# Kernel optimization log

Hardware: AMD Instinct MI355X
Metric: run time of the kernel (lower is better)

## Reference

```python
import jax, jax.numpy as jnp
import numpy as np

N_HEADS = 8
D_K = 64
SCALE = D_K ** (-0.5)


def setup_inputs() -> dict:
    key = jax.random.key(0)
    k1, k2, k3 = jax.random.split(key, 3)
    B, C, H, W = 8, 512, 32, 32
    x = jax.random.normal(k1, (B, C, H, W), dtype=jnp.float32)
    # Linear weights stored as [in, out] so y = x @ W + b (same math as torch Linear)
    W_qkv = jax.random.normal(k2, (C, N_HEADS * D_K * 3), dtype=jnp.float32) * (1.0 / np.sqrt(C))
    b_qkv = jnp.zeros((N_HEADS * D_K * 3,), dtype=jnp.float32)
    W_out = jax.random.normal(k3, (N_HEADS * D_K, C), dtype=jnp.float32) * (1.0 / np.sqrt(N_HEADS * D_K))
    b_out = jnp.zeros((C,), dtype=jnp.float32)
    return {"x": x, "W_qkv": W_qkv, "b_qkv": b_qkv, "W_out": W_out, "b_out": b_out}


def reference(x, W_qkv, b_qkv, W_out, b_out):
    B, C, H, W = x.shape
    N = H * W
    # [B, C, H, W] -> [B, N, C]  (tokens are spatial positions)
    xf = jnp.transpose(x.reshape(B, C, N), (0, 2, 1))
    # NOTE: the original forward never applies self.norm, so neither do we.
    qkv = xf @ W_qkv + b_qkv                       # [B, N, 3*h*d]
    qkv = qkv.reshape(B, N, N_HEADS, 3 * D_K)
    q, k, v = jnp.split(qkv, 3, axis=-1)           # each [B, N, h, d]
    attn = jnp.einsum('bihd,bjhd->bijh', q, k) * SCALE
    attn = jax.nn.softmax(attn, axis=2)            # softmax over key index j
    res = jnp.einsum('bijh,bjhd->bihd', attn, v)   # [B, N, h, d]
    res = res.reshape(B, N, N_HEADS * D_K)
    res = res @ W_out + b_out
    res = res + xf                                 # residual
    res = jnp.transpose(res, (0, 2, 1)).reshape(B, C, H, W)
    return res
```

## Files before the change

### kernel.cpp

```cpp
#include <hip/hip_runtime.h>
#include <hip/hip_bf16.h>
#include <cstdint>

typedef __bf16 bf16;
typedef __attribute__((ext_vector_type(8))) __bf16 bf16x8;
typedef __attribute__((ext_vector_type(4))) __bf16 bf16x4;
typedef __attribute__((ext_vector_type(4))) float f32x4;

#define CEXP 0.1803368801111244f

__global__ __launch_bounds__(256) void prep_k(const float* __restrict__ x,
                                              const float* __restrict__ Wqkv,
                                              const float* __restrict__ Wout,
                                              bf16* __restrict__ xT,
                                              bf16* __restrict__ WqkvT,
                                              bf16* __restrict__ WoutT) {
  __shared__ bf16 t[32][33];
  const int z = blockIdx.z;
  const float* src;
  bf16* dst;
  int R, C;
  if (z < 8) {
    if (blockIdx.x >= 32) return;
    src = x + (size_t)z * 512 * 1024;
    dst = xT + (size_t)z * 1024 * 512;
    R = 512; C = 1024;
  } else if (z == 8) {
    src = Wqkv; dst = WqkvT; R = 512; C = 1536;
  } else {
    if (blockIdx.x >= 16) return;
    src = Wout; dst = WoutT; R = 512; C = 512;
  }
  const int c0 = blockIdx.x * 32, r0 = blockIdx.y * 32;
  const int tx = threadIdx.x, ty = threadIdx.y;
#pragma unroll
  for (int i = 0; i < 4; ++i)
    t[ty + i * 8][tx] = (bf16)src[(size_t)(r0 + ty + i * 8) * C + c0 + tx];
  __syncthreads();
#pragma unroll
  for (int i = 0; i < 4; ++i)
    dst[(size_t)(c0 + ty + i * 8) * R + r0 + tx] = t[tx][ty + i * 8];
}

__global__ __launch_bounds__(256) void gemm_qkv(const bf16* __restrict__ xT,
                                                const bf16* __restrict__ WqkvT,
                                                const float* __restrict__ bqkv,
                                                bf16* __restrict__ Qb,
                                                bf16* __restrict__ Kb,
                                                bf16* __restrict__ Vb) {
  __shared__ bf16 As[128 * 64];
  __shared__ bf16 Bs[128 * 64];
  const int b = blockIdx.z;
  const int m0 = blockIdx.y * 128;
  const int co0 = blockIdx.x * 128;
  const int tid = threadIdx.x;
  const int w = tid >> 6, l = tid & 63;
  const int wr = w >> 1, wc = w & 1;
  const int quad = l >> 4, l16 = l & 15;

  const bf16* A = xT + (size_t)b * 1024 * 512;

  f32x4 acc[4][4];
#pragma unroll
  for (int i = 0; i < 4; ++i)
#pragma unroll
    for (int j = 0; j < 4; ++j) acc[i][j] = (f32x4){0.f, 0.f, 0.f, 0.f};

  const int srow = w * 32 + (l >> 3);
  const int scol = (l & 7) * 8;

  for (int kk = 0; kk < 8; ++kk) {
    const int k0 = kk * 64;
    bf16x8 av[4], bv[4];
#pragma unroll
    for (int i = 0; i < 4; ++i) {
      av[i] = *(const bf16x8*)&A[(size_t)(m0 + srow + i * 8) * 512 + k0 + scol];
      bv[i] = *(const bf16x8*)&WqkvT[(size_t)(co0 + srow + i * 8) * 512 + k0 + scol];
    }
#pragma unroll
    for (int i = 0; i < 4; ++i) {
      *(bf16x8*)&As[(srow + i * 8) * 64 + scol] = av[i];
      *(bf16x8*)&Bs[(srow + i * 8) * 64 + scol] = bv[i];
    }
    __syncthreads();
#pragma unroll
    for (int ks = 0; ks < 2; ++ks) {
      bf16x8 a[4], bb[4];
#pragma unroll
      for (int rb = 0; rb < 4; ++rb)
        a[rb] = *(const bf16x8*)&As[(wr * 64 + rb * 16 + l16) * 64 + ks * 32 + quad * 8];
#pragma unroll
      for (int cb = 0; cb < 4; ++cb)
        bb[cb] = *(const bf16x8*)&Bs[(wc * 64 + cb * 16 + l16) * 64 + ks * 32 + quad * 8];
#pragma unroll
      for (int rb = 0; rb < 4; ++rb)
#pragma unroll
        for (int cb = 0; cb < 4; ++cb)
          acc[rb][cb] = __builtin_amdgcn_mfma_f32_16x16x32_bf16(a[rb], bb[cb], acc[rb][cb], 0, 0, 0);
    }
    __syncthreads();
  }

#pragma unroll
  for (int cb = 0; cb < 4; ++cb) {
    const int co = co0 + wc * 64 + cb * 16 + l16;
    const int h = co / 192;
    const int rem = co - h * 192;
    const int part = rem >> 6;
    const int dd = rem & 63;
    const float bias = bqkv[co];
    if (part == 2) {
      bf16* base = Vb + ((size_t)(b * 8 + h) * 64 + dd) * 1024;
#pragma unroll
      for (int rb = 0; rb < 4; ++rb) {
        const int n = m0 + wr * 64 + rb * 16 + quad * 4;
        f32x4 v = acc[rb][cb];
        bf16x4 ov;
#pragma unroll
        for (int r = 0; r < 4; ++r) ov[r] = (bf16)(v[r] + bias);
        *(bf16x4*)&base[n] = ov;
      }
    } else {
      const float sc = (part == 0) ? CEXP : 1.0f;
      bf16* dst = (part == 0) ? Qb : Kb;
      bf16* base = dst + ((size_t)(b * 8 + h) * 1024) * 64 + dd;
#pragma unroll
      for (int rb = 0; rb < 4; ++rb) {
        const int n = m0 + wr * 64 + rb * 16 + quad * 4;
        f32x4 v = acc[rb][cb];
#pragma unroll
        for (int r = 0; r < 4; ++r) base[(size_t)(n + r) * 64] = (bf16)((v[r] + bias) * sc);
      }
    }
  }
}

__global__ __launch_bounds__(256) void attn_k(const bf16* __restrict__ Qb,
                                              const bf16* __restrict__ Kb,
                                              const bf16* __restrict__ Vb,
                                              bf16* __restrict__ Ob) {
  __shared__ bf16 Ks[128 * 72];
  __shared__ bf16 Vs[64 * 136];
  __shared__ bf16 PQs[64 * 136];
  const int bh = blockIdx.x;
  const int b = bh >> 3, h = bh & 7;
  const int q0 = blockIdx.y * 64;
  const int tid = threadIdx.x;
  const int w = tid >> 6, l = tid & 63;
  const int quad = l >> 4, l16 = l & 15;

  const bf16* Qg = Qb + (size_t)bh * 1024 * 64;
  const bf16* Kg = Kb + (size_t)bh * 1024 * 64;
  const bf16* Vg = Vb + (size_t)bh * 64 * 1024;

  {
    const int r = tid >> 2, c = (tid & 3) * 16;
    bf16x8 v0 = *(const bf16x8*)&Qg[(size_t)(q0 + r) * 64 + c];
    bf16x8 v1 = *(const bf16x8*)&Qg[(size_t)(q0 + r) * 64 + c + 8];
    *(bf16x8*)&PQs[r * 72 + c] = v0;
    *(bf16x8*)&PQs[r * 72 + c + 8] = v1;
  }
  __syncthreads();
  bf16x8 qb[4][2];
#pragma unroll
  for (int nb = 0; nb < 4; ++nb)
#pragma unroll
    for (int ks = 0; ks < 2; ++ks)
      qb[nb][ks] = *(const bf16x8*)&PQs[(nb * 16 + l16) * 72 + ks * 32 + quad * 8];

  bf16x8 ones;
#pragma unroll
  for (int e = 0; e < 8; ++e) ones[e] = (bf16)1.0f;

  f32x4 o[4], acc_l = (f32x4){0.f, 0.f, 0.f, 0.f};
#pragma unroll
  for (int db = 0; db < 4; ++db) o[db] = (f32x4){0.f, 0.f, 0.f, 0.f};

  const int kr = tid >> 1, kc = (tid & 1) * 32;
  const int vr = tid >> 2, vc = (tid & 3) * 32;

  bf16x8 ka[4], va[4];
#pragma unroll
  for (int e = 0; e < 4; ++e) {
    ka[e] = *(const bf16x8*)&Kg[(size_t)kr * 64 + kc + e * 8];
    va[e] = *(const bf16x8*)&Vg[(size_t)vr * 1024 + vc + e * 8];
  }

  for (int kv = 0; kv < 8; ++kv) {
    __syncthreads();
#pragma unroll
    for (int e = 0; e < 4; ++e) {
      *(bf16x8*)&Ks[kr * 72 + kc + e * 8] = ka[e];
      *(bf16x8*)&Vs[vr * 136 + vc + e * 8] = va[e];
    }
    __syncthreads();
    if (kv < 7) {
      const int j0 = (kv + 1) * 128;
#pragma unroll
      for (int e = 0; e < 4; ++e) {
        ka[e] = *(const bf16x8*)&Kg[(size_t)(j0 + kr) * 64 + kc + e * 8];
        va[e] = *(const bf16x8*)&Vg[(size_t)vr * 1024 + j0 + vc + e * 8];
      }
    }

    f32x4 s[4][2];
#pragma unroll
    for (int nb = 0; nb < 4; ++nb)
#pragma unroll
      for (int jb = 0; jb < 2; ++jb) s[nb][jb] = (f32x4){0.f, 0.f, 0.f, 0.f};
#pragma unroll
    for (int ks = 0; ks < 2; ++ks) {
      bf16x8 kaf[2];
#pragma unroll
      for (int jb = 0; jb < 2; ++jb)
        kaf[jb] = *(const bf16x8*)&Ks[(w * 32 + jb * 16 + l16) * 72 + ks * 32 + quad * 8];
#pragma unroll
      for (int nb = 0; nb < 4; ++nb)
#pragma unroll
        for (int jb = 0; jb < 2; ++jb)
          s[nb][jb] = __builtin_amdgcn_mfma_f32_16x16x32_bf16(kaf[jb], qb[nb][ks], s[nb][jb], 0, 0, 0);
    }

#pragma unroll
    for (int nb = 0; nb < 4; ++nb)
#pragma unroll
      for (int jb = 0; jb < 2; ++jb) {
        bf16x4 pk;
#pragma unroll
        for (int rr = 0; rr < 4; ++rr) pk[rr] = (bf16)__builtin_amdgcn_exp2f(s[nb][jb][rr]);
        *(bf16x4*)&PQs[(nb * 16 + l16) * 136 + w * 32 + jb * 16 + quad * 4] = pk;
      }
    __syncthreads();

#pragma unroll
    for (int kj = 0; kj < 4; ++kj) {
      bf16x8 ap = *(const bf16x8*)&PQs[(w * 16 + l16) * 136 + kj * 32 + quad * 8];
      acc_l = __builtin_amdgcn_mfma_f32_16x16x32_bf16(ap, ones, acc_l, 0, 0, 0);
#pragma unroll
      for (int db = 0; db < 4; ++db) {
        bf16x8 bv = *(const bf16x8*)&Vs[(db * 16 + l16) * 136 + kj * 32 + quad * 8];
        o[db] = __builtin_amdgcn_mfma_f32_16x16x32_bf16(ap, bv, o[db], 0, 0, 0);
      }
    }
  }

  f32x4 inv;
#pragma unroll
  for (int rr = 0; rr < 4; ++rr) inv[rr] = 1.0f / acc_l[rr];
  bf16* Og = Ob + (size_t)b * 1024 * 512 + h * 64;
#pragma unroll
  for (int db = 0; db < 4; ++db)
#pragma unroll
    for (int rr = 0; rr < 4; ++rr) {
      const int n = q0 + w * 16 + quad * 4 + rr;
      Og[(size_t)n * 512 + db * 16 + l16] = (bf16)(o[db][rr] * inv[rr]);
    }
}

__global__ __launch_bounds__(256) void gemm_out(const bf16* __restrict__ Ob,
                                                const bf16* __restrict__ WoutT,
                                                const float* __restrict__ bout,
                                                const float* __restrict__ x,
                                                float* __restrict__ out) {
  __shared__ bf16 As[128 * 64];
  __shared__ bf16 Bs[128 * 64];
  const int b = blockIdx.z;
  const int m0 = blockIdx.y * 128;
  const int co0 = blockIdx.x * 128;
  const int tid = threadIdx.x;
  const int w = tid >> 6, l = tid & 63;
  const int wr = w >> 1, wc = w & 1;
  const int quad = l >> 4, l16 = l & 15;

  const bf16* A = Ob + (size_t)b * 1024 * 512;

  f32x4 acc[4][4];
#pragma unroll
  for (int i = 0; i < 4; ++i)
#pragma unroll
    for (int j = 0; j < 4; ++j) acc[i][j] = (f32x4){0.f, 0.f, 0.f, 0.f};

  const int srow = w * 32 + (l >> 3);
  const int scol = (l & 7) * 8;

  for (int kk = 0; kk < 8; ++kk) {
    const int k0 = kk * 64;
    bf16x8 av[4], bv[4];
#pragma unroll
    for (int i = 0; i < 4; ++i) {
      av[i] = *(const bf16x8*)&A[(size_t)(m0 + srow + i * 8) * 512 + k0 + scol];
      bv[i] = *(const bf16x8*)&WoutT[(size_t)(co0 + srow + i * 8) * 512 + k0 + scol];
    }
#pragma unroll
    for (int i = 0; i < 4; ++i) {
      *(bf16x8*)&As[(srow + i * 8) * 64 + scol] = av[i];
      *(bf16x8*)&Bs[(srow + i * 8) * 64 + scol] = bv[i];
    }
    __syncthreads();
#pragma unroll
    for (int ks = 0; ks < 2; ++ks) {
      bf16x8 a[4], bb[4];
#pragma unroll
      for (int rb = 0; rb < 4; ++rb)
        a[rb] = *(const bf16x8*)&As[(wr * 64 + rb * 16 + l16) * 64 + ks * 32 + quad * 8];
#pragma unroll
      for (int cb = 0; cb < 4; ++cb)
        bb[cb] = *(const bf16x8*)&Bs[(wc * 64 + cb * 16 + l16) * 64 + ks * 32 + quad * 8];
#pragma unroll
      for (int rb = 0; rb < 4; ++rb)
#pragma unroll
        for (int cb = 0; cb < 4; ++cb)
          acc[rb][cb] = __builtin_amdgcn_mfma_f32_16x16x32_bf16(a[rb], bb[cb], acc[rb][cb], 0, 0, 0);
    }
    __syncthreads();
  }

#pragma unroll
  for (int cb = 0; cb < 4; ++cb) {
    const int c = co0 + wc * 64 + cb * 16 + l16;
    const float bias = bout[c];
#pragma unroll
    for (int rb = 0; rb < 4; ++rb) {
      const int n = m0 + wr * 64 + rb * 16 + quad * 4;
      const size_t off = ((size_t)b * 512 + c) * 1024 + n;
      f32x4 res = *(const f32x4*)&x[off];
      f32x4 v = acc[rb][cb];
      f32x4 ov;
#pragma unroll
      for (int r = 0; r < 4; ++r) ov[r] = v[r] + bias + res[r];
      *(f32x4*)&out[off] = ov;
    }
  }
}

extern "C" void kernel_launch(void* const* d_in, const int* in_sizes, int n_in,
                              void* d_out, int out_size, void* d_ws, size_t ws_size,
                              hipStream_t stream) {
  const float* x = (const float*)d_in[0];
  const float* Wqkv = (const float*)d_in[1];
  const float* bqkv = (const float*)d_in[2];
  const float* Wout = (const float*)d_in[3];
  const float* bout = (const float*)d_in[4];
  float* out = (float*)d_out;
  char* ws = (char*)d_ws;

  const size_t MB = 1024 * 1024;
  bf16* xT = (bf16*)(ws);
  bf16* Ob = xT;
  bf16* Qbuf = (bf16*)(ws + 8 * MB);
  bf16* Kbuf = (bf16*)(ws + 16 * MB);
  bf16* Vbuf = (bf16*)(ws + 24 * MB);
  bf16* WqkvT = (bf16*)(ws + 32 * MB);
  bf16* WoutT = (bf16*)(ws + 32 * MB + 1572864);
  if (ws_size < 32 * MB + 1572864 + 524288) return;

  prep_k<<<dim3(48, 16, 10), dim3(32, 8), 0, stream>>>(x, Wqkv, Wout, xT, WqkvT, WoutT);
  gemm_qkv<<<dim3(12, 8, 8), 256, 0, stream>>>(xT, WqkvT, bqkv, Qbuf, Kbuf, Vbuf);
  attn_k<<<dim3(64, 16), 256, 0, stream>>>(Qbuf, Kbuf, Vbuf, Ob);
  gemm_out<<<dim3(4, 8, 8), 256, 0, stream>>>(Ob, WoutT, bout, x, out);
}
```

Before: 159.3 us.

## Fuse x transpose into QKV GEMM, widen attention query tile, pad LDS

The QKV GEMM now reads fp32 x directly in channel-major layout, converts it to bf16 and writes it transposed into a swizzled LDS tile. This removes the separate transpose pass over x and its workspace round trip. Each attention block now handles 128 queries instead of 64, so every K/V tile loaded from global memory is reused across twice as many queries, at the cost of more registers and LDS and half as many blocks. The GEMM LDS rows are also padded from 64 to 72 elements to reduce bank conflicts.

```diff
diff --git a/kernel.cpp b/kernel.cpp
--- a/kernel.cpp
+++ b/kernel.cpp
@@ -9,10 +9,8 @@
 
 #define CEXP 0.1803368801111244f
 
-__global__ __launch_bounds__(256) void prep_k(const float* __restrict__ x,
-                                              const float* __restrict__ Wqkv,
+__global__ __launch_bounds__(256) void prep_k(const float* __restrict__ Wqkv,
                                               const float* __restrict__ Wout,
-                                              bf16* __restrict__ xT,
                                               bf16* __restrict__ WqkvT,
                                               bf16* __restrict__ WoutT) {
   __shared__ bf16 t[32][33];
@@ -20,12 +18,7 @@
   const float* src;
   bf16* dst;
   int R, C;
-  if (z < 8) {
-    if (blockIdx.x >= 32) return;
-    src = x + (size_t)z * 512 * 1024;
-    dst = xT + (size_t)z * 1024 * 512;
-    R = 512; C = 1024;
-  } else if (z == 8) {
+  if (z == 0) {
     src = Wqkv; dst = WqkvT; R = 512; C = 1536;
   } else {
     if (blockIdx.x >= 16) return;
@@ -42,14 +35,14 @@
     dst[(size_t)(c0 + ty + i * 8) * R + r0 + tx] = t[tx][ty + i * 8];
 }
 
-__global__ __launch_bounds__(256) void gemm_qkv(const bf16* __restrict__ xT,
+__global__ __launch_bounds__(256) void gemm_qkv(const float* __restrict__ x,
                                                 const bf16* __restrict__ WqkvT,
                                                 const float* __restrict__ bqkv,
                                                 bf16* __restrict__ Qb,
                                                 bf16* __restrict__ Kb,
                                                 bf16* __restrict__ Vb) {
-  __shared__ bf16 As[128 * 64];
-  __shared__ bf16 Bs[128 * 64];
+  __shared__ bf16 As[128 * 72];
+  __shared__ bf16 Bs[128 * 72];
   const int b = blockIdx.z;
   const int m0 = blockIdx.y * 128;
   const int co0 = blockIdx.x * 128;
@@ -58,7 +51,7 @@
   const int wr = w >> 1, wc = w & 1;
   const int quad = l >> 4, l16 = l & 15;
 
-  const bf16* A = xT + (size_t)b * 1024 * 512;
+  const float* Xb = x + (size_t)b * 512 * 1024;
 
   f32x4 acc[4][4];
 #pragma unroll
@@ -66,32 +59,43 @@
 #pragma unroll
     for (int j = 0; j < 4; ++j) acc[i][j] = (f32x4){0.f, 0.f, 0.f, 0.f};
 
+  const int nl = (tid & 31) * 4;
+  const int cl0 = tid >> 5;
   const int srow = w * 32 + (l >> 3);
   const int scol = (l & 7) * 8;
 
   for (int kk = 0; kk < 8; ++kk) {
     const int k0 = kk * 64;
-    bf16x8 av[4], bv[4];
-#pragma unroll
-    for (int i = 0; i < 4; ++i) {
-      av[i] = *(const bf16x8*)&A[(size_t)(m0 + srow + i * 8) * 512 + k0 + scol];
+    f32x4 xa[8];
+    bf16x8 bv[4];
+#pragma unroll
+    for (int p = 0; p < 8; ++p)
+      xa[p] = *(const f32x4*)&Xb[(size_t)(k0 + cl0 + p * 8) * 1024 + m0 + nl];
+#pragma unroll
+    for (int i = 0; i < 4; ++i)
       bv[i] = *(const bf16x8*)&WqkvT[(size_t)(co0 + srow + i * 8) * 512 + k0 + scol];
-    }
-#pragma unroll
-    for (int i = 0; i < 4; ++i) {
-      *(bf16x8*)&As[(srow + i * 8) * 64 + scol] = av[i];
-      *(bf16x8*)&Bs[(srow + i * 8) * 64 + scol] = bv[i];
-    }
+#pragma unroll
+    for (int p = 0; p < 8; ++p)
+#pragma unroll
+      for (int i = 0; i < 4; ++i) {
+        const int n = nl + i;
+        As[n * 72 + ((p ^ ((n >> 2) & 7)) << 3) + cl0] = (bf16)xa[p][i];
+      }
+#pragma unroll
+    for (int i = 0; i < 4; ++i)
+      *(bf16x8*)&Bs[(srow + i * 8) * 72 + scol] = bv[i];
     __syncthreads();
 #pragma unroll
     for (int ks = 0; ks < 2; ++ks) {
       bf16x8 a[4], bb[4];
 #pragma unroll
-      for (int rb = 0; rb < 4; ++rb)
-        a[rb] = *(const bf16x8*)&As[(wr * 64 + rb * 16 + l16) * 64 + ks * 32 + quad * 8];
+      for (int rb = 0; rb < 4; ++rb) {
+        const int m = wr * 64 + rb * 16 + l16;
+        a[rb] = *(const bf16x8*)&As[m * 72 + (((ks * 4 + quad) ^ ((m >> 2) & 7)) << 3)];
+      }
 #pragma unroll
       for (int cb = 0; cb < 4; ++cb)
-        bb[cb] = *(const bf16x8*)&Bs[(wc * 64 + cb * 16 + l16) * 64 + ks * 32 + quad * 8];
+        bb[cb] = *(const bf16x8*)&Bs[(wc * 64 + cb * 16 + l16) * 72 + ks * 32 + quad * 8];
 #pragma unroll
       for (int rb = 0; rb < 4; ++rb)
 #pragma unroll
@@ -141,10 +145,10 @@
                                               bf16* __restrict__ Ob) {
   __shared__ bf16 Ks[128 * 72];
   __shared__ bf16 Vs[64 * 136];
-  __shared__ bf16 PQs[64 * 136];
+  __shared__ bf16 PQs[128 * 136];
   const int bh = blockIdx.x;
   const int b = bh >> 3, h = bh & 7;
-  const int q0 = blockIdx.y * 64;
+  const int q0 = blockIdx.y * 128;
   const int tid = threadIdx.x;
   const int w = tid >> 6, l = tid & 63;
   const int quad = l >> 4, l16 = l & 15;
@@ -154,16 +158,16 @@
   const bf16* Vg = Vb + (size_t)bh * 64 * 1024;
 
   {
-    const int r = tid >> 2, c = (tid & 3) * 16;
-    bf16x8 v0 = *(const bf16x8*)&Qg[(size_t)(q0 + r) * 64 + c];
-    bf16x8 v1 = *(const bf16x8*)&Qg[(size_t)(q0 + r) * 64 + c + 8];
-    *(bf16x8*)&PQs[r * 72 + c] = v0;
-    *(bf16x8*)&PQs[r * 72 + c + 8] = v1;
+    const int r = tid >> 1, c = (tid & 1) * 32;
+#pragma unroll
+    for (int e = 0; e < 4; ++e)
+      *(bf16x8*)&PQs[r * 72 + c + e * 8] =
+          *(const bf16x8*)&Qg[(size_t)(q0 + r) * 64 + c + e * 8];
   }
   __syncthreads();
-  bf16x8 qb[4][2];
-#pragma unroll
-  for (int nb = 0; nb < 4; ++nb)
+  bf16x8 qb[8][2];
+#pragma unroll
+  for (int nb = 0; nb < 8; ++nb)
 #pragma unroll
     for (int ks = 0; ks < 2; ++ks)
       qb[nb][ks] = *(const bf16x8*)&PQs[(nb * 16 + l16) * 72 + ks * 32 + quad * 8];
@@ -172,9 +176,13 @@
 #pragma unroll
   for (int e = 0; e < 8; ++e) ones[e] = (bf16)1.0f;
 
-  f32x4 o[4], acc_l = (f32x4){0.f, 0.f, 0.f, 0.f};
-#pragma unroll
-  for (int db = 0; db < 4; ++db) o[db] = (f32x4){0.f, 0.f, 0.f, 0.f};
+  f32x4 o[2][4], acc_l[2];
+#pragma unroll
+  for (int mt = 0; mt < 2; ++mt) {
+    acc_l[mt] = (f32x4){0.f, 0.f, 0.f, 0.f};
+#pragma unroll
+    for (int db = 0; db < 4; ++db) o[mt][db] = (f32x4){0.f, 0.f, 0.f, 0.f};
+  }
 
   const int kr = tid >> 1, kc = (tid & 1) * 32;
   const int vr = tid >> 2, vc = (tid & 3) * 32;
@@ -203,9 +211,9 @@
       }
     }
 
-    f32x4 s[4][2];
-#pragma unroll
-    for (int nb = 0; nb < 4; ++nb)
+    f32x4 s[8][2];
+#pragma unroll
+    for (int nb = 0; nb < 8; ++nb)
 #pragma unroll
       for (int jb = 0; jb < 2; ++jb) s[nb][jb] = (f32x4){0.f, 0.f, 0.f, 0.f};
 #pragma unroll
@@ -215,14 +223,14 @@
       for (int jb = 0; jb < 2; ++jb)
         kaf[jb] = *(const bf16x8*)&Ks[(w * 32 + jb * 16 + l16) * 72 + ks * 32 + quad * 8];
 #pragma unroll
-      for (int nb = 0; nb < 4; ++nb)
+      for (int nb = 0; nb < 8; ++nb)
 #pragma unroll
         for (int jb = 0; jb < 2; ++jb)
           s[nb][jb] = __builtin_amdgcn_mfma_f32_16x16x32_bf16(kaf[jb], qb[nb][ks], s[nb][jb], 0, 0, 0);
     }
 
 #pragma unroll
-    for (int nb = 0; nb < 4; ++nb)
+    for (int nb = 0; nb < 8; ++nb)
 #pragma unroll
       for (int jb = 0; jb < 2; ++jb) {
         bf16x4 pk;
@@ -234,27 +242,36 @@
 
 #pragma unroll
     for (int kj = 0; kj < 4; ++kj) {
-      bf16x8 ap = *(const bf16x8*)&PQs[(w * 16 + l16) * 136 + kj * 32 + quad * 8];
-      acc_l = __builtin_amdgcn_mfma_f32_16x16x32_bf16(ap, ones, acc_l, 0, 0, 0);
+      bf16x8 ap[2];
+#pragma unroll
+      for (int mt = 0; mt < 2; ++mt) {
+        ap[mt] = *(const bf16x8*)&PQs[(w * 32 + mt * 16 + l16) * 136 + kj * 32 + quad * 8];
+        acc_l[mt] = __builtin_amdgcn_mfma_f32_16x16x32_bf16(ap[mt], ones, acc_l[mt], 0, 0, 0);
+      }
 #pragma unroll
       for (int db = 0; db < 4; ++db) {
         bf16x8 bv = *(const bf16x8*)&Vs[(db * 16 + l16) * 136 + kj * 32 + quad * 8];
-        o[db] = __builtin_amdgcn_mfma_f32_16x16x32_bf16(ap, bv, o[db], 0, 0, 0);
-      }
-    }
-  }
-
-  f32x4 inv;
-#pragma unroll
-  for (int rr = 0; rr < 4; ++rr) inv[rr] = 1.0f / acc_l[rr];
+#pragma unroll
+        for (int mt = 0; mt < 2; ++mt)
+          o[mt][db] = __builtin_amdgcn_mfma_f32_16x16x32_bf16(ap[mt], bv, o[mt][db], 0, 0, 0);
+      }
+    }
+  }
+
   bf16* Og = Ob + (size_t)b * 1024 * 512 + h * 64;
 #pragma unroll
-  for (int db = 0; db < 4; ++db)
-#pragma unroll
-    for (int rr = 0; rr < 4; ++rr) {
-      const int n = q0 + w * 16 + quad * 4 + rr;
-      Og[(size_t)n * 512 + db * 16 + l16] = (bf16)(o[db][rr] * inv[rr]);
-    }
+  for (int mt = 0; mt < 2; ++mt) {
+    f32x4 inv;
+#pragma unroll
+    for (int rr = 0; rr < 4; ++rr) inv[rr] = 1.0f / acc_l[mt][rr];
+#pragma unroll
+    for (int db = 0; db < 4; ++db)
+#pragma unroll
+      for (int rr = 0; rr < 4; ++rr) {
+        const int n = q0 + w * 32 + mt * 16 + quad * 4 + rr;
+        Og[(size_t)n * 512 + db * 16 + l16] = (bf16)(o[mt][db][rr] * inv[rr]);
+      }
+  }
 }
 
 __global__ __launch_bounds__(256) void gemm_out(const bf16* __restrict__ Ob,
@@ -262,8 +279,8 @@
                                                 const float* __restrict__ bout,
                                                 const float* __restrict__ x,
                                                 float* __restrict__ out) {
-  __shared__ bf16 As[128 * 64];
-  __shared__ bf16 Bs[128 * 64];
+  __shared__ bf16 As[128 * 72];
+  __shared__ bf16 Bs[128 * 72];
   const int b = blockIdx.z;
   const int m0 = blockIdx.y * 128;
   const int co0 = blockIdx.x * 128;
@@ -293,8 +310,8 @@
     }
 #pragma unroll
     for (int i = 0; i < 4; ++i) {
-      *(bf16x8*)&As[(srow + i * 8) * 64 + scol] = av[i];
-      *(bf16x8*)&Bs[(srow + i * 8) * 64 + scol] = bv[i];
+      *(bf16x8*)&As[(srow + i * 8) * 72 + scol] = av[i];
+      *(bf16x8*)&Bs[(srow + i * 8) * 72 + scol] = bv[i];
     }
     __syncthreads();
 #pragma unroll
@@ -302,10 +319,10 @@
       bf16x8 a[4], bb[4];
 #pragma unroll
       for (int rb = 0; rb < 4; ++rb)
-        a[rb] = *(const bf16x8*)&As[(wr * 64 + rb * 16 + l16) * 64 + ks * 32 + quad * 8];
+        a[rb] = *(const bf16x8*)&As[(wr * 64 + rb * 16 + l16) * 72 + ks * 32 + quad * 8];
 #pragma unroll
       for (int cb = 0; cb < 4; ++cb)
-        bb[cb] = *(const bf16x8*)&Bs[(wc * 64 + cb * 16 + l16) * 64 + ks * 32 + quad * 8];
+        bb[cb] = *(const bf16x8*)&Bs[(wc * 64 + cb * 16 + l16) * 72 + ks * 32 + quad * 8];
 #pragma unroll
       for (int rb = 0; rb < 4; ++rb)
 #pragma unroll
@@ -345,8 +362,7 @@
   char* ws = (char*)d_ws;
 
   const size_t MB = 1024 * 1024;
-  bf16* xT = (bf16*)(ws);
-  bf16* Ob = xT;
+  bf16* Ob = (bf16*)(ws);
   bf16* Qbuf = (bf16*)(ws + 8 * MB);
   bf16* Kbuf = (bf16*)(ws + 16 * MB);
   bf16* Vbuf = (bf16*)(ws + 24 * MB);
@@ -354,8 +370,8 @@
   bf16* WoutT = (bf16*)(ws + 32 * MB + 1572864);
   if (ws_size < 32 * MB + 1572864 + 524288) return;
 
-  prep_k<<<dim3(48, 16, 10), dim3(32, 8), 0, stream>>>(x, Wqkv, Wout, xT, WqkvT, WoutT);
-  gemm_qkv<<<dim3(12, 8, 8), 256, 0, stream>>>(xT, WqkvT, bqkv, Qbuf, Kbuf, Vbuf);
-  attn_k<<<dim3(64, 16), 256, 0, stream>>>(Qbuf, Kbuf, Vbuf, Ob);
+  prep_k<<<dim3(48, 16, 2), dim3(32, 8), 0, stream>>>(Wqkv, Wout, WqkvT, WoutT);
+  gemm_qkv<<<dim3(12, 8, 8), 256, 0, stream>>>(x, WqkvT, bqkv, Qbuf, Kbuf, Vbuf);
+  attn_k<<<dim3(64, 8), 256, 0, stream>>>(Qbuf, Kbuf, Vbuf, Ob);
   gemm_out<<<dim3(4, 8, 8), 256, 0, stream>>>(Ob, WoutT, bout, x, out);
 }
```

New measurement: 154.9 us. 1.03x faster.
